# Kernel tuning notes

Measured on AMD Instinct MI355X. Metric: run time of the kernel, lower is better.

The kernel has to match this reference:

```python
import jax, jax.numpy as jnp
import numpy as np

NEG_SLOPE = 0.01  # torch nn.LeakyReLU default

N_NODES = 100000
N_EDGES = 1000000
D_FEAT = 64


def setup_inputs() -> dict:
    key = jax.random.key(0)
    ks = jax.random.split(key, 8)
    x = jax.random.normal(ks[0], (N_NODES, D_FEAT), dtype=jnp.float32)
    src = jax.random.randint(ks[1], (N_EDGES,), 0, N_NODES, dtype=jnp.int64 if jax.config.jax_enable_x64 else jnp.int32)
    dst = jax.random.randint(ks[2], (N_EDGES,), 0, N_NODES, dtype=jnp.int64 if jax.config.jax_enable_x64 else jnp.int32)
    s = 1.0 / np.sqrt(D_FEAT)
    W1 = jax.random.normal(ks[3], (D_FEAT, 64), dtype=jnp.float32) * s
    b1 = jnp.zeros((64,), dtype=jnp.float32)
    W2 = jax.random.normal(ks[4], (64, 64), dtype=jnp.float32) * s
    b2 = jnp.zeros((64,), dtype=jnp.float32)
    Wc = jax.random.normal(ks[5], (64, 2), dtype=jnp.float32) * s
    bc = jnp.zeros((2,), dtype=jnp.float32)
    return {"x": x, "src": src, "dst": dst, "W1": W1, "b1": b1,
            "W2": W2, "b2": b2, "Wc": Wc, "bc": bc}


def _graph_conv(x, src, dst, W, b, out_deg_isqrt, in_deg_isqrt, n_nodes):
    # DGL GraphConv, norm='both': h_v = ( sum_{u->v} x_u / sqrt(d_out(u)) ) / sqrt(d_in(v)) @ W + b
    # (in_feats <= out_feats here, so aggregate first then transform, matching DGL order)
    h = x * out_deg_isqrt[:, None]          # [N, d] scale by source out-degree
    msg = h[src]                            # [E, d] gather
    agg = jax.ops.segment_sum(msg, dst, num_segments=n_nodes)  # [N, d] scatter-add
    agg = agg * in_deg_isqrt[:, None]
    return agg @ W + b


def reference(x, src, dst, W1, b1, W2, b2, Wc, bc):
    n = x.shape[0]
    ones_e = jnp.ones(src.shape[0], dtype=x.dtype)
    out_deg = jnp.clip(jax.ops.segment_sum(ones_e, src, num_segments=n), 1.0)
    in_deg = jnp.clip(jax.ops.segment_sum(ones_e, dst, num_segments=n), 1.0)
    out_isqrt = out_deg ** -0.5
    in_isqrt = in_deg ** -0.5

    h = _graph_conv(x, src, dst, W1, b1, out_isqrt, in_isqrt, n)
    h = jax.nn.leaky_relu(h, NEG_SLOPE)
    h = _graph_conv(h, src, dst, W2, b2, out_isqrt, in_isqrt, n)
    h = jax.nn.leaky_relu(h, NEG_SLOPE)
    return h @ Wc + bc  # prediction=True -> linear classifier
```

## Files before the change

kernel.cpp:

```cpp
#include <hip/hip_runtime.h>


typedef __attribute__((ext_vector_type(8))) short short8;
typedef __attribute__((ext_vector_type(4))) float f32x4;

#define NPB 256
#define SEG 64
#define BSH 9
#define BW  512

__device__ __forceinline__ float b2f(unsigned short u) {
    return __uint_as_float(((unsigned int)u) << 16);
}
__device__ __forceinline__ unsigned short f2b(float f) {
    unsigned int i = __float_as_uint(f);
    unsigned int r = (i + 0x7FFFu + ((i >> 16) & 1u)) >> 16;
    return (unsigned short)r;
}

__device__ __forceinline__ void acc8(float* a, short8 f) {
    int4 d = *(int4*)&f;
#pragma unroll
    for (int q = 0; q < 4; q++) {
        unsigned int dw = (unsigned int)((q == 0) ? d.x : (q == 1) ? d.y
                                       : (q == 2) ? d.z : d.w);
        a[2 * q]     += __uint_as_float(dw << 16);
        a[2 * q + 1] += __uint_as_float(dw & 0xFFFF0000u);
    }
}

__global__ __launch_bounds__(1024) void count_kernel(
    const int* __restrict__ src, const int* __restrict__ dst,
    int* __restrict__ cntD, int* __restrict__ cntS, int e, int chunk) {
    __shared__ int hD[256], hS[256];
    int t = threadIdx.x, pb = blockIdx.x;
    if (t < 256) { hD[t] = 0; hS[t] = 0; }
    __syncthreads();
    int e0 = pb * chunk, e1 = min(e, e0 + chunk);
    for (int i = e0 + 4 * t; i + 3 < e1; i += 4096) {
        int4 d4 = *(const int4*)(dst + i);
        int4 s4 = *(const int4*)(src + i);
        atomicAdd(&hD[d4.x >> BSH], 1);
        atomicAdd(&hD[d4.y >> BSH], 1);
        atomicAdd(&hD[d4.z >> BSH], 1);
        atomicAdd(&hD[d4.w >> BSH], 1);
        atomicAdd(&hS[s4.x >> BSH], 1);
        atomicAdd(&hS[s4.y >> BSH], 1);
        atomicAdd(&hS[s4.z >> BSH], 1);
        atomicAdd(&hS[s4.w >> BSH], 1);
    }
    int tb0 = e0 + ((e1 - e0) & ~3);
    for (int i = tb0 + t; i < e1; i += 1024) {
        atomicAdd(&hD[dst[i] >> BSH], 1);
        atomicAdd(&hS[src[i] >> BSH], 1);
    }
    __syncthreads();
    if (t < 256) {
        cntD[t * NPB + pb] = hD[t];
        cntS[t * NPB + pb] = hS[t];
    }
}

__global__ __launch_bounds__(1024) void scanmat_kernel(int* __restrict__ cntD,
                                                       int* __restrict__ cntS) {
    int* a = (blockIdx.x == 0) ? cntD : cntS;
    int4* a4 = (int4*)a;
    __shared__ int s[1024];
    int t = threadIdx.x;
    int4 v[SEG / 4];
    int sum = 0;
#pragma unroll
    for (int j = 0; j < SEG / 4; j++) {
        v[j] = a4[t * (SEG / 4) + j];
        sum += v[j].x + v[j].y + v[j].z + v[j].w;
    }
    s[t] = sum;
    __syncthreads();
    for (int d = 1; d < 1024; d <<= 1) {
        int x = (t >= d) ? s[t - d] : 0;
        __syncthreads();
        s[t] += x;
        __syncthreads();
    }
    int run = s[t] - sum;
#pragma unroll
    for (int j = 0; j < SEG / 4; j++) {
        int p0 = run;
        int p1 = p0 + v[j].x;
        int p2 = p1 + v[j].y;
        int p3 = p2 + v[j].z;
        run = p3 + v[j].w;
        a4[t * (SEG / 4) + j] = make_int4(p0, p1, p2, p3);
    }
}

__global__ __launch_bounds__(1024) void part_kernel(
    const int* __restrict__ src, const int* __restrict__ dst,
    const int* __restrict__ cntD, const int* __restrict__ cntS,
    unsigned int* __restrict__ ebuf, unsigned short* __restrict__ sbuf,
    int e, int chunk) {
    __shared__ int cD[256], cS[256];
    int t = threadIdx.x, pb = blockIdx.x;
    if (t < 256) {
        cD[t] = cntD[t * NPB + pb];
        cS[t] = cntS[t * NPB + pb];
    }
    __syncthreads();
    int e0 = pb * chunk, e1 = min(e, e0 + chunk);
    for (int i = e0 + 4 * t; i + 3 < e1; i += 4096) {
        int4 d4 = *(const int4*)(dst + i);
        int4 s4 = *(const int4*)(src + i);
#pragma unroll
        for (int k = 0; k < 4; k++) {
            int s_ = (k == 0) ? s4.x : (k == 1) ? s4.y : (k == 2) ? s4.z : s4.w;
            int d_ = (k == 0) ? d4.x : (k == 1) ? d4.y : (k == 2) ? d4.z : d4.w;
            int pd = atomicAdd(&cD[d_ >> BSH], 1);
            ebuf[pd] = ((unsigned int)s_ << BSH) | (unsigned int)(d_ & (BW - 1));
            int ps_ = atomicAdd(&cS[s_ >> BSH], 1);
            sbuf[ps_] = (unsigned short)(s_ & (BW - 1));
        }
    }
    int tb0 = e0 + ((e1 - e0) & ~3);
    for (int i = tb0 + t; i < e1; i += 1024) {
        int s_ = src[i], d_ = dst[i];
        int pd = atomicAdd(&cD[d_ >> BSH], 1);
        ebuf[pd] = ((unsigned int)s_ << BSH) | (unsigned int)(d_ & (BW - 1));
        int ps_ = atomicAdd(&cS[s_ >> BSH], 1);
        sbuf[ps_] = (unsigned short)(s_ & (BW - 1));
    }
}

__global__ __launch_bounds__(512) void bucket_kernel(
    const unsigned int* __restrict__ ebuf, const unsigned short* __restrict__ sbuf,
    const int* __restrict__ cntD, const int* __restrict__ cntS,
    int* __restrict__ row, int* __restrict__ lenp,
    float* __restrict__ ii, float* __restrict__ oi,
    int* __restrict__ csr, int n, int e) {
    __shared__ int cnt[BW], cur[BW], ocnt[BW], ps[BW];
    int t = threadIdx.x, b = blockIdx.x;
    int v0 = b << BSH;
    int eb0 = cntD[b * NPB], eb1 = cntD[(b + 1) * NPB];
    int sb0 = cntS[b * NPB], sb1 = cntS[(b + 1) * NPB];
    int pbase = ((eb0 + 7) & ~7) + (v0 << 3);
    cnt[t] = 0; ocnt[t] = 0;
    __syncthreads();
    for (int i = eb0 + t; i < eb1; i += 512)
        atomicAdd(&cnt[ebuf[i] & (BW - 1)], 1);
    for (int i = sb0 + t; i < sb1; i += 512)
        atomicAdd(&ocnt[sbuf[i]], 1);
    __syncthreads();
    int c = cnt[t];
    int p = (c + 7) & ~7;
    ps[t] = p;
    __syncthreads();
    for (int d = 1; d < 512; d <<= 1) {
        int x = (t >= d) ? ps[t - d] : 0;
        __syncthreads();
        ps[t] += x;
        __syncthreads();
    }
    int pexcl = ps[t] - p;
    cur[t] = pexcl;
    int v = v0 + t;
    if (v < n) {
        row[v] = pbase + pexcl;
        lenp[v] = p;
        ii[v] = rsqrtf((float)max(c, 1));
        oi[v] = rsqrtf((float)max(ocnt[t], 1));
    }
    __syncthreads();
    for (int i = eb0 + t; i < eb1; i += 512) {
        unsigned int pk = ebuf[i];
        int r = atomicAdd(&cur[pk & (BW - 1)], 1);
        csr[pbase + r] = (int)(pk >> BSH);
    }
    if (v < n)
        for (int k = c; k < p; k++) csr[pbase + pexcl + k] = n;
}

__global__ __launch_bounds__(256) void xconv_kernel(
    const float4* __restrict__ x4, const float* __restrict__ oi,
    ushort4* __restrict__ xb, ushort4* __restrict__ h1b4, int total4) {
    int idx = blockIdx.x * blockDim.x + threadIdx.x;
    int stride = gridDim.x * blockDim.x;
    for (int i = idx; i < total4; i += stride) {
        float s = oi[i >> 4];
        float4 val = x4[i];
        xb[i] = make_ushort4(f2b(val.x * s), f2b(val.y * s),
                             f2b(val.z * s), f2b(val.w * s));
    }
    if (idx < 16) {
        xb[total4 + idx] = make_ushort4(0, 0, 0, 0);
        h1b4[total4 + idx] = make_ushort4(0, 0, 0, 0);
    }
}

template <bool FINAL>
__global__ __launch_bounds__(256) void fused_kernel(
    const short8* __restrict__ featb, const int* __restrict__ row,
    const int* __restrict__ lenp, const int* __restrict__ csr,
    const float* __restrict__ ii, const float* __restrict__ oi,
    const float* __restrict__ W, const float* __restrict__ bias,
    const float* __restrict__ Wc, const float* __restrict__ bcl,
    void* __restrict__ out, int n, int nwaves) {
    __shared__ short8 tile[4][16 * 9];
    int lane = threadIdx.x & 63;
    int o = lane >> 3, s = lane & 7;
    int m15 = lane & 15, quad = lane >> 4;
    short8* tl = tile[threadIdx.x >> 6];
    int wid = blockIdx.x * (blockDim.x >> 6) + (threadIdx.x >> 6);
    int ngroups = (n + 15) >> 4;

    short8 bf[4][2];
#pragma unroll
    for (int nt = 0; nt < 4; nt++)
#pragma unroll
        for (int kk = 0; kk < 2; kk++)
#pragma unroll
            for (int j = 0; j < 8; j++)
                bf[nt][kk][j] = (short)f2b(W[(kk * 32 + quad * 8 + j) * 64 + nt * 16 + m15]);

    float bias_r[4];
#pragma unroll
    for (int nt = 0; nt < 4; nt++) bias_r[nt] = bias[nt * 16 + m15];

    float wc_r[4][2];
    float bc0 = 0.f, bc1 = 0.f;
    if constexpr (FINAL) {
#pragma unroll
        for (int nt = 0; nt < 4; nt++) {
            wc_r[nt][0] = Wc[(nt * 16 + m15) * 2];
            wc_r[nt][1] = Wc[(nt * 16 + m15) * 2 + 1];
        }
        bc0 = bcl[0];
        bc1 = bcl[1];
    }

    for (int g = wid; g < ngroups; g += nwaves) {
        int rbase = g << 4;

        int vA = rbase + o, vB = rbase + 8 + o;
        bool valA = vA < n, valB = vB < n;
        int baseA = 0, pcA = 0, baseB = 0, pcB = 0;
        if (valA) { baseA = row[vA]; pcA = lenp[vA]; }
        if (valB) { baseB = row[vB]; pcB = lenp[vB]; }
        float aA[8], aB[8];
#pragma unroll
        for (int k = 0; k < 8; k++) { aA[k] = 0.f; aB[k] = 0.f; }
        int jA = 0, jB = 0;
        while (jA < pcA || jB < pcB) {
            bool dA = jA < pcA, dB = jB < pcB;
            int4 uA0, uA1, uB0, uB1;
            short8 fA0, fA1, fA2, fA3, fA4, fA5, fA6, fA7;
            short8 fB0, fB1, fB2, fB3, fB4, fB5, fB6, fB7;
            if (dA) {
                uA0 = *(const int4*)(csr + baseA + jA);
                uA1 = *(const int4*)(csr + baseA + jA + 4);
            }
            if (dB) {
                uB0 = *(const int4*)(csr + baseB + jB);
                uB1 = *(const int4*)(csr + baseB + jB + 4);
            }
            if (dA) {
                fA0 = featb[(size_t)uA0.x * 8 + s];
                fA1 = featb[(size_t)uA0.y * 8 + s];
                fA2 = featb[(size_t)uA0.z * 8 + s];
                fA3 = featb[(size_t)uA0.w * 8 + s];
                fA4 = featb[(size_t)uA1.x * 8 + s];
                fA5 = featb[(size_t)uA1.y * 8 + s];
                fA6 = featb[(size_t)uA1.z * 8 + s];
                fA7 = featb[(size_t)uA1.w * 8 + s];
            }
            if (dB) {
                fB0 = featb[(size_t)uB0.x * 8 + s];
                fB1 = featb[(size_t)uB0.y * 8 + s];
                fB2 = featb[(size_t)uB0.z * 8 + s];
                fB3 = featb[(size_t)uB0.w * 8 + s];
                fB4 = featb[(size_t)uB1.x * 8 + s];
                fB5 = featb[(size_t)uB1.y * 8 + s];
                fB6 = featb[(size_t)uB1.z * 8 + s];
                fB7 = featb[(size_t)uB1.w * 8 + s];
            }
            if (dA) {
                acc8(aA, fA0); acc8(aA, fA1); acc8(aA, fA2); acc8(aA, fA3);
                acc8(aA, fA4); acc8(aA, fA5); acc8(aA, fA6); acc8(aA, fA7);
                jA += 8;
            }
            if (dB) {
                acc8(aB, fB0); acc8(aB, fB1); acc8(aB, fB2); acc8(aB, fB3);
                acc8(aB, fB4); acc8(aB, fB5); acc8(aB, fB6); acc8(aB, fB7);
                jB += 8;
            }
        }
        float iivA = valA ? ii[vA] : 0.f;
        float iivB = valB ? ii[vB] : 0.f;
        short8 rA, rB;
#pragma unroll
        for (int m = 0; m < 8; m++) {
            rA[m] = (short)f2b(aA[m] * iivA);
            rB[m] = (short)f2b(aB[m] * iivB);
        }
        tl[o * 9 + s] = rA;
        tl[(8 + o) * 9 + s] = rB;

        short8 af0 = tl[m15 * 9 + quad];
        short8 af1 = tl[m15 * 9 + 4 + quad];

        f32x4 acc[4];
#pragma unroll
        for (int nt = 0; nt < 4; nt++) {
            f32x4 z = {0.f, 0.f, 0.f, 0.f};
            z = __builtin_amdgcn_mfma_f32_16x16x32_bf16(af0, bf[nt][0], z, 0, 0, 0);
            z = __builtin_amdgcn_mfma_f32_16x16x32_bf16(af1, bf[nt][1], z, 0, 0, 0);
            acc[nt] = z;
        }

        if constexpr (!FINAL) {
#pragma unroll
            for (int r = 0; r < 4; r++) {
                int vr = rbase + quad * 4 + r;
                float os = (vr < n) ? oi[vr] : 0.f;
#pragma unroll
                for (int nt = 0; nt < 4; nt++) {
                    float ov = acc[nt][r] + bias_r[nt];
                    ov = (ov > 0.f) ? ov : 0.01f * ov;
                    if (vr < n)
                        ((unsigned short*)out)[(size_t)vr * 64 + nt * 16 + m15] = f2b(ov * os);
                }
            }
        } else {
#pragma unroll
            for (int r = 0; r < 4; r++) {
                float p0 = 0.f, p1 = 0.f;
#pragma unroll
                for (int nt = 0; nt < 4; nt++) {
                    float ov = acc[nt][r] + bias_r[nt];
                    ov = (ov > 0.f) ? ov : 0.01f * ov;
                    p0 = fmaf(ov, wc_r[nt][0], p0);
                    p1 = fmaf(ov, wc_r[nt][1], p1);
                }
#pragma unroll
                for (int off = 1; off < 16; off <<= 1) {
                    p0 += __shfl_xor(p0, off);
                    p1 += __shfl_xor(p1, off);
                }
                int vr = rbase + quad * 4 + r;
                if (m15 == 0 && vr < n)
                    ((float2*)out)[vr] = make_float2(p0 + bc0, p1 + bc1);
            }
        }
    }
}

extern "C" void kernel_launch(void* const* d_in, const int* in_sizes, int n_in,
                              void* d_out, int out_size, void* d_ws, size_t ws_size,
                              hipStream_t stream) {
    const float* x  = (const float*)d_in[0];
    const int* src  = (const int*)d_in[1];
    const int* dst  = (const int*)d_in[2];
    const float* W1 = (const float*)d_in[3];
    const float* b1 = (const float*)d_in[4];
    const float* W2 = (const float*)d_in[5];
    const float* b2 = (const float*)d_in[6];
    const float* Wc = (const float*)d_in[7];
    const float* bc = (const float*)d_in[8];
    int n = in_sizes[0] / 64;
    int e = in_sizes[1];
    int total = n * 64;
    int nbuck = (n + BW - 1) >> BSH;

    char* ws = (char*)d_ws;
    size_t off = 0;
    auto take = [&](size_t bytes) -> char* {
        char* p = ws + off;
        off = (off + bytes + 255) & ~(size_t)255;
        return p;
    };
    int* cntD = (int*)take(256 * NPB * 4);
    int* cntS = (int*)take(256 * NPB * 4);
    unsigned int* ebuf = (unsigned int*)take((size_t)e * 4);
    unsigned short* sbuf = (unsigned short*)take((size_t)e * 2);
    int* row  = (int*)take((size_t)(n + 1) * 4);
    int* lenp = (int*)take((size_t)n * 4);
    int* csr  = (int*)take(((size_t)e + 8 * (size_t)nbuck * BW + 16) * 4);
    float* oi = (float*)take((size_t)n * 4);
    float* ii = (float*)take((size_t)n * 4);
    unsigned short* xb  = (unsigned short*)take((size_t)(total + 64) * 2);
    unsigned short* h1b = (unsigned short*)take((size_t)(total + 64) * 2);

    int chunk = (((e + NPB - 1) / NPB) + 3) & ~3;

    count_kernel<<<NPB, 1024, 0, stream>>>(src, dst, cntD, cntS, e, chunk);
    scanmat_kernel<<<2, 1024, 0, stream>>>(cntD, cntS);
    part_kernel<<<NPB, 1024, 0, stream>>>(src, dst, cntD, cntS, ebuf, sbuf, e, chunk);
    bucket_kernel<<<nbuck, 512, 0, stream>>>(ebuf, sbuf, cntD, cntS,
                                             row, lenp, ii, oi, csr, n, e);
    xconv_kernel<<<2048, 256, 0, stream>>>((const float4*)x, oi, (ushort4*)xb,
                                           (ushort4*)h1b, n * 16);

    const int fblocks = 1568;
    const int fwaves = fblocks * (256 / 64);

    fused_kernel<false><<<fblocks, 256, 0, stream>>>((const short8*)xb, row, lenp, csr,
                                                     ii, oi, W1, b1, nullptr, nullptr,
                                                     h1b, n, fwaves);
    fused_kernel<true><<<fblocks, 256, 0, stream>>>((const short8*)h1b, row, lenp, csr,
                                                    ii, nullptr, W2, b2, Wc, bc,
                                                    d_out, n, fwaves);
}
```

Before: 203.4 us.

## Split aggregation from GEMM and store features in column-quarter planes

Node features are now stored as four planes of 16 bf16 columns each, and the fused gather+MFMA kernel is split into a separate aggregation kernel and a GEMM kernel. The aggregation kernel runs four passes, one per column plane, with four lanes splitting each node's edges and combining partial sums by shuffle. The aim is to keep each pass's gathered working set (about 3.2 MB) small enough to stay cache-resident and to give the gather more parallelism. The cost is an extra round trip of the aggregated features through global memory, two more kernel launches, and four rereads of the CSR index lists.

Measured after the change: 227.6 us. 11.9% more time.

```diff
diff --git a/kernel.cpp b/kernel.cpp
--- a/kernel.cpp
+++ b/kernel.cpp
@@ -180,34 +180,91 @@
 
 __global__ __launch_bounds__(256) void xconv_kernel(
     const float4* __restrict__ x4, const float* __restrict__ oi,
-    ushort4* __restrict__ xb, ushort4* __restrict__ h1b4, int total4) {
+    ushort4* __restrict__ xq, ushort4* __restrict__ h1q, int n) {
     int idx = blockIdx.x * blockDim.x + threadIdx.x;
     int stride = gridDim.x * blockDim.x;
+    int total4 = n * 16;
     for (int i = idx; i < total4; i += stride) {
-        float s = oi[i >> 4];
+        int v = i >> 4, c4 = i & 15;
+        int q = c4 >> 2;
+        float s = oi[v];
         float4 val = x4[i];
-        xb[i] = make_ushort4(f2b(val.x * s), f2b(val.y * s),
-                             f2b(val.z * s), f2b(val.w * s));
+        xq[((size_t)q * (n + 1) + v) * 4 + (c4 & 3)] =
+            make_ushort4(f2b(val.x * s), f2b(val.y * s),
+                         f2b(val.z * s), f2b(val.w * s));
     }
     if (idx < 16) {
-        xb[total4 + idx] = make_ushort4(0, 0, 0, 0);
-        h1b4[total4 + idx] = make_ushort4(0, 0, 0, 0);
+        int q = idx >> 2, j = idx & 3;
+        xq[((size_t)q * (n + 1) + n) * 4 + j] = make_ushort4(0, 0, 0, 0);
+        h1q[((size_t)q * (n + 1) + n) * 4 + j] = make_ushort4(0, 0, 0, 0);
+    }
+}
+
+__global__ __launch_bounds__(256) void aggq_kernel(
+    const short8* __restrict__ featq, const int* __restrict__ row,
+    const int* __restrict__ lenp, const int* __restrict__ csr,
+    const float* __restrict__ ii, short8* __restrict__ aggq,
+    int n, int bpp) {
+    int b = blockIdx.x;
+    int pass = b / bpp, bp = b - pass * bpp;
+    int lane = threadIdx.x & 63;
+    int o = lane >> 3, k = (lane >> 1) & 3, h = lane & 1;
+    int wave = threadIdx.x >> 6;
+    int v = (bp * 4 + wave) * 8 + o;
+    bool valid = v < n;
+    int base = 0, pc = 0;
+    if (valid) { base = row[v]; pc = lenp[v]; }
+    size_t qoff = (size_t)pass * (n + 1) * 2;
+    float a[8];
+#pragma unroll
+    for (int m = 0; m < 8; m++) a[m] = 0.f;
+    int j = 0;
+    for (; j + 15 < pc; j += 16) {
+        int4 u0 = *(const int4*)(csr + base + j);
+        int4 u1 = *(const int4*)(csr + base + j + 4);
+        int4 u2 = *(const int4*)(csr + base + j + 8);
+        int4 u3 = *(const int4*)(csr + base + j + 12);
+        int e0 = (k == 0) ? u0.x : (k == 1) ? u0.y : (k == 2) ? u0.z : u0.w;
+        int e1 = (k == 0) ? u1.x : (k == 1) ? u1.y : (k == 2) ? u1.z : u1.w;
+        int e2 = (k == 0) ? u2.x : (k == 1) ? u2.y : (k == 2) ? u2.z : u2.w;
+        int e3 = (k == 0) ? u3.x : (k == 1) ? u3.y : (k == 2) ? u3.z : u3.w;
+        short8 f0 = featq[qoff + (size_t)e0 * 2 + h];
+        short8 f1 = featq[qoff + (size_t)e1 * 2 + h];
+        short8 f2 = featq[qoff + (size_t)e2 * 2 + h];
+        short8 f3 = featq[qoff + (size_t)e3 * 2 + h];
+        acc8(a, f0); acc8(a, f1); acc8(a, f2); acc8(a, f3);
+    }
+    if (j < pc) {
+        int4 u0 = *(const int4*)(csr + base + j);
+        int4 u1 = *(const int4*)(csr + base + j + 4);
+        int e0 = (k == 0) ? u0.x : (k == 1) ? u0.y : (k == 2) ? u0.z : u0.w;
+        int e1 = (k == 0) ? u1.x : (k == 1) ? u1.y : (k == 2) ? u1.z : u1.w;
+        short8 f0 = featq[qoff + (size_t)e0 * 2 + h];
+        short8 f1 = featq[qoff + (size_t)e1 * 2 + h];
+        acc8(a, f0); acc8(a, f1);
+    }
+#pragma unroll
+    for (int m = 0; m < 8; m++) {
+        a[m] += __shfl_xor(a[m], 2);
+        a[m] += __shfl_xor(a[m], 4);
+    }
+    if (valid && k == 0) {
+        float iiv = ii[v];
+        short8 r;
+#pragma unroll
+        for (int m = 0; m < 8; m++) r[m] = (short)f2b(a[m] * iiv);
+        aggq[qoff + (size_t)v * 2 + h] = r;
     }
 }
 
 template <bool FINAL>
-__global__ __launch_bounds__(256) void fused_kernel(
-    const short8* __restrict__ featb, const int* __restrict__ row,
-    const int* __restrict__ lenp, const int* __restrict__ csr,
-    const float* __restrict__ ii, const float* __restrict__ oi,
+__global__ __launch_bounds__(256) void gemm_kernel(
+    const short8* __restrict__ aggq, const float* __restrict__ oi,
     const float* __restrict__ W, const float* __restrict__ bias,
     const float* __restrict__ Wc, const float* __restrict__ bcl,
     void* __restrict__ out, int n, int nwaves) {
-    __shared__ short8 tile[4][16 * 9];
     int lane = threadIdx.x & 63;
-    int o = lane >> 3, s = lane & 7;
     int m15 = lane & 15, quad = lane >> 4;
-    short8* tl = tile[threadIdx.x >> 6];
     int wid = blockIdx.x * (blockDim.x >> 6) + (threadIdx.x >> 6);
     int ngroups = (n + 15) >> 4;
 
@@ -238,73 +295,10 @@
 
     for (int g = wid; g < ngroups; g += nwaves) {
         int rbase = g << 4;
-
-        int vA = rbase + o, vB = rbase + 8 + o;
-        bool valA = vA < n, valB = vB < n;
-        int baseA = 0, pcA = 0, baseB = 0, pcB = 0;
-        if (valA) { baseA = row[vA]; pcA = lenp[vA]; }
-        if (valB) { baseB = row[vB]; pcB = lenp[vB]; }
-        float aA[8], aB[8];
-#pragma unroll
-        for (int k = 0; k < 8; k++) { aA[k] = 0.f; aB[k] = 0.f; }
-        int jA = 0, jB = 0;
-        while (jA < pcA || jB < pcB) {
-            bool dA = jA < pcA, dB = jB < pcB;
-            int4 uA0, uA1, uB0, uB1;
-            short8 fA0, fA1, fA2, fA3, fA4, fA5, fA6, fA7;
-            short8 fB0, fB1, fB2, fB3, fB4, fB5, fB6, fB7;
-            if (dA) {
-                uA0 = *(const int4*)(csr + baseA + jA);
-                uA1 = *(const int4*)(csr + baseA + jA + 4);
-            }
-            if (dB) {
-                uB0 = *(const int4*)(csr + baseB + jB);
-                uB1 = *(const int4*)(csr + baseB + jB + 4);
-            }
-            if (dA) {
-                fA0 = featb[(size_t)uA0.x * 8 + s];
-                fA1 = featb[(size_t)uA0.y * 8 + s];
-                fA2 = featb[(size_t)uA0.z * 8 + s];
-                fA3 = featb[(size_t)uA0.w * 8 + s];
-                fA4 = featb[(size_t)uA1.x * 8 + s];
-                fA5 = featb[(size_t)uA1.y * 8 + s];
-                fA6 = featb[(size_t)uA1.z * 8 + s];
-                fA7 = featb[(size_t)uA1.w * 8 + s];
-            }
-            if (dB) {
-                fB0 = featb[(size_t)uB0.x * 8 + s];
-                fB1 = featb[(size_t)uB0.y * 8 + s];
-                fB2 = featb[(size_t)uB0.z * 8 + s];
-                fB3 = featb[(size_t)uB0.w * 8 + s];
-                fB4 = featb[(size_t)uB1.x * 8 + s];
-                fB5 = featb[(size_t)uB1.y * 8 + s];
-                fB6 = featb[(size_t)uB1.z * 8 + s];
-                fB7 = featb[(size_t)uB1.w * 8 + s];
-            }
-            if (dA) {
-                acc8(aA, fA0); acc8(aA, fA1); acc8(aA, fA2); acc8(aA, fA3);
-                acc8(aA, fA4); acc8(aA, fA5); acc8(aA, fA6); acc8(aA, fA7);
-                jA += 8;
-            }
-            if (dB) {
-                acc8(aB, fB0); acc8(aB, fB1); acc8(aB, fB2); acc8(aB, fB3);
-                acc8(aB, fB4); acc8(aB, fB5); acc8(aB, fB6); acc8(aB, fB7);
-                jB += 8;
-            }
-        }
-        float iivA = valA ? ii[vA] : 0.f;
-        float iivB = valB ? ii[vB] : 0.f;
-        short8 rA, rB;
-#pragma unroll
-        for (int m = 0; m < 8; m++) {
-            rA[m] = (short)f2b(aA[m] * iivA);
-            rB[m] = (short)f2b(aB[m] * iivB);
-        }
-        tl[o * 9 + s] = rA;
-        tl[(8 + o) * 9 + s] = rB;
-
-        short8 af0 = tl[m15 * 9 + quad];
-        short8 af1 = tl[m15 * 9 + 4 + quad];
+        int rm = min(rbase + m15, n - 1);
+
+        short8 af0 = aggq[((size_t)(quad >> 1) * (n + 1) + rm) * 2 + (quad & 1)];
+        short8 af1 = aggq[((size_t)((4 + quad) >> 1) * (n + 1) + rm) * 2 + (quad & 1)];
 
         f32x4 acc[4];
 #pragma unroll
@@ -325,7 +319,8 @@
                     float ov = acc[nt][r] + bias_r[nt];
                     ov = (ov > 0.f) ? ov : 0.01f * ov;
                     if (vr < n)
-                        ((unsigned short*)out)[(size_t)vr * 64 + nt * 16 + m15] = f2b(ov * os);
+                        ((unsigned short*)out)[((size_t)nt * (n + 1) + vr) * 16 + m15]
+                            = f2b(ov * os);
                 }
             }
         } else {
@@ -366,7 +361,6 @@
     const float* bc = (const float*)d_in[8];
     int n = in_sizes[0] / 64;
     int e = in_sizes[1];
-    int total = n * 64;
     int nbuck = (n + BW - 1) >> BSH;
 
     char* ws = (char*)d_ws;
@@ -385,8 +379,9 @@
     int* csr  = (int*)take(((size_t)e + 8 * (size_t)nbuck * BW + 16) * 4);
     float* oi = (float*)take((size_t)n * 4);
     float* ii = (float*)take((size_t)n * 4);
-    unsigned short* xb  = (unsigned short*)take((size_t)(total + 64) * 2);
-    unsigned short* h1b = (unsigned short*)take((size_t)(total + 64) * 2);
+    unsigned short* xq   = (unsigned short*)take((size_t)(n + 1) * 64 * 2);
+    unsigned short* h1q  = (unsigned short*)take((size_t)(n + 1) * 64 * 2);
+    unsigned short* aggb = (unsigned short*)take((size_t)(n + 1) * 64 * 2);
 
     int chunk = (((e + NPB - 1) / NPB) + 3) & ~3;
 
@@ -395,16 +390,22 @@
     part_kernel<<<NPB, 1024, 0, stream>>>(src, dst, cntD, cntS, ebuf, sbuf, e, chunk);
     bucket_kernel<<<nbuck, 512, 0, stream>>>(ebuf, sbuf, cntD, cntS,
                                              row, lenp, ii, oi, csr, n, e);
-    xconv_kernel<<<2048, 256, 0, stream>>>((const float4*)x, oi, (ushort4*)xb,
-                                           (ushort4*)h1b, n * 16);
-
-    const int fblocks = 1568;
-    const int fwaves = fblocks * (256 / 64);
-
-    fused_kernel<false><<<fblocks, 256, 0, stream>>>((const short8*)xb, row, lenp, csr,
-                                                     ii, oi, W1, b1, nullptr, nullptr,
-                                                     h1b, n, fwaves);
-    fused_kernel<true><<<fblocks, 256, 0, stream>>>((const short8*)h1b, row, lenp, csr,
-                                                    ii, nullptr, W2, b2, Wc, bc,
-                                                    d_out, n, fwaves);
-}
+    xconv_kernel<<<2048, 256, 0, stream>>>((const float4*)x, oi, (ushort4*)xq,
+                                           (ushort4*)h1q, n);
+
+    int bpp = (n + 31) / 32;
+    int agrid = 4 * bpp;
+    const int gblocks = 512;
+    const int gwaves = gblocks * (256 / 64);
+
+    aggq_kernel<<<agrid, 256, 0, stream>>>((const short8*)xq, row, lenp, csr,
+                                           ii, (short8*)aggb, n, bpp);
+    gemm_kernel<false><<<gblocks, 256, 0, stream>>>((const short8*)aggb, oi,
+                                                    W1, b1, nullptr, nullptr,
+                                                    h1q, n, gwaves);
+    aggq_kernel<<<agrid, 256, 0, stream>>>((const short8*)h1q, row, lenp, csr,
+                                           ii, (short8*)aggb, n, bpp);
+    gemm_kernel<true><<<gblocks, 256, 0, stream>>>((const short8*)aggb, nullptr,
+                                                   W2, b2, Wc, bc,
+                                                   d_out, n, gwaves);
+}
```
